# Optimization experiments

Hardware: AMD Instinct MI355X
Metric: run time of the kernel (lower is better)

The kernel has to match this reference:

```python
import jax, jax.numpy as jnp
import numpy as np

COMMITMENT_COST = 0.25


def setup_inputs() -> dict:
    key = jax.random.key(0)
    k1, k2 = jax.random.split(key)
    x = jax.random.normal(k1, (4, 64, 32, 32, 32), dtype=jnp.float32)
    weight = jax.random.normal(k2, (512, 64), dtype=jnp.float32)
    return {"x": x, "weight": weight}


def reference(x, weight):
    b, c, h, w, d = x.shape  # c == embed_dim
    # [b, h, w, d, c] -> [N, c]
    flat = jnp.transpose(x, (0, 2, 3, 4, 1)).reshape(-1, c)
    # squared L2 distances to each codebook vector: [N, n_embed]
    distances = (
        jnp.sum(flat * flat, axis=1, keepdims=True)
        - 2.0 * (flat @ weight.T)
        + jnp.sum(weight * weight, axis=1)
    )
    embed_idx_flat = jnp.argmin(distances, axis=1)  # == argmax(-distances)
    embed_idx = embed_idx_flat.reshape(b, h, w, d)
    # gather codebook rows and move embed dim back to channel position
    quantized = jnp.transpose(weight[embed_idx], (0, 4, 1, 2, 3))  # [b, c, h, w, d]
    latent_loss = COMMITMENT_COST * jnp.mean(
        (jax.lax.stop_gradient(quantized) - x) ** 2
    )
    quantized_st = jax.lax.stop_gradient(quantized - x) + x
    return quantized_st, embed_idx, latent_loss
```

## Files before the change

### kernel.cpp

```cpp
#include <hip/hip_runtime.h>
#include <hip/hip_bf16.h>

#define HWD      32768
#define NC       64
#define NE       512
#define OUT_IDX  8388608
#define OUT_LOSS 8519680

#define WS_WSQ_F   16
#define WS_WP_B    4096
#define WS_NEEDED  200704

typedef __attribute__((ext_vector_type(8))) short bf16x8;
typedef __attribute__((ext_vector_type(4))) float f32x4;

__device__ inline unsigned short bf16_rne(float v) {
    unsigned u = __builtin_bit_cast(unsigned, v);
    return (unsigned short)((u + 0x7FFFu + ((u >> 16) & 1u)) >> 16);
}
__device__ inline float bf16_f(unsigned short s) {
    return __builtin_bit_cast(float, (unsigned)s << 16);
}
__device__ inline void split3(float v, unsigned short& h, unsigned short& m,
                              unsigned short& l) {
    h = bf16_rne(v);
    float r1 = v - bf16_f(h);
    m = bf16_rne(r1);
    float r2 = r1 - bf16_f(m);
    l = bf16_rne(r2);
}

__global__ __launch_bounds__(256) void vq_prep(
    const float* __restrict__ w, float* __restrict__ ws)
{
    const int gtid = blockIdx.x * 256 + threadIdx.x;
    if (gtid == 0) { ws[0] = 0.f; ((unsigned*)ws)[1] = 0u; }
    if (gtid < NE) {
        const float4* row = (const float4*)(w + (size_t)gtid * NC);
        float s0 = 0.f, s1 = 0.f, s2 = 0.f, s3 = 0.f;
#pragma unroll
        for (int k = 0; k < 16; ++k) {
            float4 v = row[k];
            s0 = fmaf(v.x, v.x, s0); s1 = fmaf(v.y, v.y, s1);
            s2 = fmaf(v.z, v.z, s2); s3 = fmaf(v.w, v.w, s3);
        }
        ws[WS_WSQ_F + gtid] = (s0 + s1) + (s2 + s3);
    }
    const int lane_s = gtid & 63;
    int t = gtid >> 6;
    const int plane = t % 3; t /= 3;
    const int kc = t & 1;
    const int ct = t >> 1;
    const int code = ct * 16 + (lane_s & 15);
    const int kb   = kc * 32 + (lane_s >> 4) * 8;
    const float* src = w + (size_t)code * NC + kb;
    unsigned short o[8];
#pragma unroll
    for (int j = 0; j < 8; ++j) {
        unsigned short h, m, l;
        split3(src[j], h, m, l);
        o[j] = (plane == 0) ? h : (plane == 1) ? m : l;
    }
    unsigned short* dst = (unsigned short*)((char*)ws + WS_WP_B) + (size_t)gtid * 8;
#pragma unroll
    for (int j = 0; j < 8; ++j) dst[j] = o[j];
}

__global__ __launch_bounds__(256, 4) void vq_fused2(
    const float* __restrict__ x, const float* __restrict__ w,
    float* __restrict__ ws, float* __restrict__ out)
{
    __shared__ float q_sh[64 * 65];
    __shared__ int   idx_sh[128];
    __shared__ float wred[4];

    const int tid    = threadIdx.x;
    const int wv     = tid >> 6;
    const int lane   = tid & 63;
    const int lanelo = lane & 15;
    const int quad   = lane >> 4;
    const int posB   = blockIdx.x * 128;
    const int b      = posB >> 15;
    const int hwdB   = posB & (HWD - 1);
    const size_t xoff = (size_t)b * NC * HWD + hwdB;
    const int wpos   = wv * 32;

    bf16x8 A[2][2][3];
    float  xsqp[2];
#pragma unroll
    for (int pt = 0; pt < 2; ++pt) {
        float xs = 0.f;
#pragma unroll
        for (int kc = 0; kc < 2; ++kc) {
            bf16x8 fh, fm, fl;
#pragma unroll
            for (int j = 0; j < 8; ++j) {
                const int k = kc * 32 + quad * 8 + j;
                const float v = x[xoff + (size_t)k * HWD + wpos + pt * 16 + lanelo];
                unsigned short h, m, l;
                split3(v, h, m, l);
                fh[j] = (short)h; fm[j] = (short)m; fl[j] = (short)l;
                xs = fmaf(v, v, xs);
            }
            A[pt][kc][0] = fh; A[pt][kc][1] = fm; A[pt][kc][2] = fl;
        }
        xs += __shfl_xor(xs, 16);
        xs += __shfl_xor(xs, 32);
        xsqp[pt] = xs;
    }
    float xsq_r[2][4];
#pragma unroll
    for (int pt = 0; pt < 2; ++pt)
#pragma unroll
        for (int r = 0; r < 4; ++r)
            xsq_r[pt][r] = __shfl(xsqp[pt], quad * 4 + r);

    const bf16x8* wp   = (const bf16x8*)((const char*)ws + WS_WP_B);
    const float*  wsqp = ws + WS_WSQ_F;

    float best[2][4];
    int   bidx[2][4];
#pragma unroll
    for (int pt = 0; pt < 2; ++pt)
#pragma unroll
        for (int r = 0; r < 4; ++r) { best[pt][r] = 3.402823466e38f; bidx[pt][r] = 0; }

    for (int ct = 0; ct < 32; ++ct) {
        bf16x8 B[2][3];
#pragma unroll
        for (int kc = 0; kc < 2; ++kc)
#pragma unroll
            for (int p = 0; p < 3; ++p)
                B[kc][p] = wp[(size_t)((ct * 2 + kc) * 3 + p) * 64 + lane];
        const float wsq_c = wsqp[ct * 16 + lanelo];

#pragma unroll
        for (int pt = 0; pt < 2; ++pt) {
            f32x4 acc = {0.f, 0.f, 0.f, 0.f};
            acc = __builtin_amdgcn_mfma_f32_16x16x32_bf16(A[pt][0][2], B[0][0], acc, 0, 0, 0);
            acc = __builtin_amdgcn_mfma_f32_16x16x32_bf16(A[pt][1][2], B[1][0], acc, 0, 0, 0);
            acc = __builtin_amdgcn_mfma_f32_16x16x32_bf16(A[pt][0][1], B[0][1], acc, 0, 0, 0);
            acc = __builtin_amdgcn_mfma_f32_16x16x32_bf16(A[pt][1][1], B[1][1], acc, 0, 0, 0);
            acc = __builtin_amdgcn_mfma_f32_16x16x32_bf16(A[pt][0][0], B[0][2], acc, 0, 0, 0);
            acc = __builtin_amdgcn_mfma_f32_16x16x32_bf16(A[pt][1][0], B[1][2], acc, 0, 0, 0);
            acc = __builtin_amdgcn_mfma_f32_16x16x32_bf16(A[pt][0][1], B[0][0], acc, 0, 0, 0);
            acc = __builtin_amdgcn_mfma_f32_16x16x32_bf16(A[pt][1][1], B[1][0], acc, 0, 0, 0);
            acc = __builtin_amdgcn_mfma_f32_16x16x32_bf16(A[pt][0][0], B[0][1], acc, 0, 0, 0);
            acc = __builtin_amdgcn_mfma_f32_16x16x32_bf16(A[pt][1][0], B[1][1], acc, 0, 0, 0);
            acc = __builtin_amdgcn_mfma_f32_16x16x32_bf16(A[pt][0][0], B[0][0], acc, 0, 0, 0);
            acc = __builtin_amdgcn_mfma_f32_16x16x32_bf16(A[pt][1][0], B[1][0], acc, 0, 0, 0);
#pragma unroll
            for (int r = 0; r < 4; ++r) {
                const float d = fmaf(-2.f, acc[r], xsq_r[pt][r]) + wsq_c;
                const int ge = ct * 16 + lanelo;
                if (d < best[pt][r]) { best[pt][r] = d; bidx[pt][r] = ge; }
            }
        }
    }

#pragma unroll
    for (int pt = 0; pt < 2; ++pt)
#pragma unroll
        for (int r = 0; r < 4; ++r) {
            float d = best[pt][r]; int i = bidx[pt][r];
#pragma unroll
            for (int mlane = 1; mlane <= 8; mlane <<= 1) {
                const float d2 = __shfl_xor(d, mlane);
                const int   i2 = __shfl_xor(i, mlane);
                if (d2 < d || (d2 == d && i2 < i)) { d = d2; i = i2; }
            }
            if (lanelo == 0)
                idx_sh[wpos + pt * 16 + quad * 4 + r] = i;
        }
    __syncthreads();

    if (tid < 128) out[OUT_IDX + posB + tid] = (float)idx_sh[tid];

    float lsum = 0.f;
#pragma unroll 1
    for (int rnd = 0; rnd < 2; ++rnd) {
        if (rnd) __syncthreads();
#pragma unroll
        for (int it = 0; it < 16; ++it) {
            const int e = it * 256 + tid;
            const int r = e >> 6, c = e & 63;
            q_sh[r * 65 + c] = w[(size_t)idx_sh[rnd * 64 + r] * NC + c];
        }
        __syncthreads();
#pragma unroll
        for (int it = 0; it < 16; ++it) {
            const int e = it * 256 + tid;
            const int c = e >> 6;
            const int p = e & 63;
            const size_t off = xoff + (size_t)c * HWD + rnd * 64 + p;
            const float xv = x[off];
            const float q  = q_sh[p * 65 + c];
            const float dq = q - xv;
            lsum = fmaf(dq, dq, lsum);
            out[off] = dq + xv;
        }
    }

#pragma unroll
    for (int off = 32; off >= 1; off >>= 1) lsum += __shfl_down(lsum, off);
    if (lane == 0) wred[wv] = lsum;
    __syncthreads();
    if (tid == 0) {
        atomicAdd((float*)ws, (wred[0] + wred[1]) + (wred[2] + wred[3]));
        __threadfence();
        const unsigned done = atomicAdd((unsigned*)ws + 1, 1u);
        if (done == 1023u) {
            const float L = atomicAdd((float*)ws, 0.f);
            out[OUT_LOSS] = 0.25f * L / 8388608.0f;
        }
    }
}

__global__ __launch_bounds__(256, 2) void vq_fused_fb(
    const float* __restrict__ x, const float* __restrict__ w,
    float* __restrict__ out, float* __restrict__ loss_acc)
{
    __shared__ float lw[256 * NC];
    __shared__ float wsq[256];
    __shared__ float wred[4];
    const int tid = threadIdx.x;
    const int n0  = blockIdx.x * 512;
    const int b   = n0 >> 15;
    const int hwd = (n0 & (HWD - 1)) + tid;
    const float* xp = x + (size_t)b * NC * HWD + hwd;
    float xr0[NC], xr1[NC];
#pragma unroll
    for (int c = 0; c < NC; ++c) { xr0[c] = xp[(size_t)c * HWD]; xr1[c] = xp[(size_t)c * HWD + 256]; }
    float xsq0 = 0.f, xsq1 = 0.f;
#pragma unroll
    for (int c = 0; c < NC; ++c) { xsq0 = fmaf(xr0[c], xr0[c], xsq0); xsq1 = fmaf(xr1[c], xr1[c], xsq1); }
    float best0 = 3.402823466e38f, best1 = 3.402823466e38f;
    int bi0 = 0, bi1 = 0;
    for (int pass = 0; pass < 2; ++pass) {
        if (pass) __syncthreads();
        const float4* wt = (const float4*)(w + pass * 256 * NC);
        float4* l4 = (float4*)lw;
#pragma unroll
        for (int k = 0; k < 16; ++k) l4[tid + k * 256] = wt[tid + k * 256];
        {
            const float4* row = wt + tid * 16;
            float s0 = 0.f, s1 = 0.f, s2 = 0.f, s3 = 0.f;
#pragma unroll
            for (int k = 0; k < 16; ++k) {
                float4 v = row[k];
                s0 = fmaf(v.x, v.x, s0); s1 = fmaf(v.y, v.y, s1);
                s2 = fmaf(v.z, v.z, s2); s3 = fmaf(v.w, v.w, s3);
            }
            wsq[tid] = (s0 + s1) + (s2 + s3);
        }
        __syncthreads();
#pragma unroll 2
        for (int e = 0; e < 256; ++e) {
            const float4* row = (const float4*)(lw + e * NC);
            float a0 = 0.f, a1 = 0.f, c0 = 0.f, c1 = 0.f;
#pragma unroll
            for (int k = 0; k < 16; ++k) {
                float4 v = row[k];
                a0 = fmaf(xr0[4 * k + 0], v.x, a0); a1 = fmaf(xr0[4 * k + 1], v.y, a1);
                a0 = fmaf(xr0[4 * k + 2], v.z, a0); a1 = fmaf(xr0[4 * k + 3], v.w, a1);
                c0 = fmaf(xr1[4 * k + 0], v.x, c0); c1 = fmaf(xr1[4 * k + 1], v.y, c1);
                c0 = fmaf(xr1[4 * k + 2], v.z, c0); c1 = fmaf(xr1[4 * k + 3], v.w, c1);
            }
            const float d0 = (xsq0 - 2.f * (a0 + a1)) + wsq[e];
            const float d1 = (xsq1 - 2.f * (c0 + c1)) + wsq[e];
            const int ge = pass * 256 + e;
            if (d0 < best0) { best0 = d0; bi0 = ge; }
            if (d1 < best1) { best1 = d1; bi1 = ge; }
        }
    }
    float* o0 = out + (size_t)b * NC * HWD + hwd;
    float lsum = 0.f;
    const float4* r0 = (const float4*)(w + bi0 * NC);
    const float4* r1 = (const float4*)(w + bi1 * NC);
#pragma unroll
    for (int k = 0; k < 16; ++k) {
        float4 q0 = r0[k], q1 = r1[k];
        float qv0[4] = { q0.x, q0.y, q0.z, q0.w };
        float qv1[4] = { q1.x, q1.y, q1.z, q1.w };
#pragma unroll
        for (int j = 0; j < 4; ++j) {
            const int c = 4 * k + j;
            const float dv0 = qv0[j] - xr0[c];
            const float dv1 = qv1[j] - xr1[c];
            lsum = fmaf(dv0, dv0, lsum); lsum = fmaf(dv1, dv1, lsum);
            o0[(size_t)c * HWD] = dv0 + xr0[c];
            o0[(size_t)c * HWD + 256] = dv1 + xr1[c];
        }
    }
    const int n = b * HWD + hwd;
    out[OUT_IDX + n] = (float)bi0;
    out[OUT_IDX + n + 256] = (float)bi1;
#pragma unroll
    for (int off = 32; off >= 1; off >>= 1) lsum += __shfl_down(lsum, off);
    if ((tid & 63) == 0) wred[tid >> 6] = lsum;
    __syncthreads();
    if (tid == 0) atomicAdd(loss_acc, (wred[0] + wred[1]) + (wred[2] + wred[3]));
}

__global__ void vq_loss_fin_fb(const float* __restrict__ acc, float* __restrict__ out)
{
    out[OUT_LOSS] = 0.25f * acc[0] / 8388608.0f;
}

extern "C" void kernel_launch(void* const* d_in, const int* in_sizes, int n_in,
                              void* d_out, int out_size, void* d_ws, size_t ws_size,
                              hipStream_t stream)
{
    const float* x = (const float*)d_in[0];
    const float* w = (const float*)d_in[1];
    float* out = (float*)d_out;
    float* ws  = (float*)d_ws;

    if (ws_size >= WS_NEEDED) {
        vq_prep<<<48, 256, 0, stream>>>(w, ws);
        vq_fused2<<<1024, 256, 0, stream>>>(x, w, ws, out);
    } else {
        hipMemsetAsync(d_ws, 0, sizeof(float), stream);
        vq_fused_fb<<<256, 256, 0, stream>>>(x, w, out, ws);
        vq_loss_fin_fb<<<1, 1, 0, stream>>>(ws, out);
    }
}
```

Measured before the change: 162.0 us.

## Double-buffer codebook tile loads and drop per-row x-norm from argmin

The codebook-tile loop now uses two register buffers, loading the next tile's B fragments and weight norms while the MFMA chain on the current tile runs, so global-load latency overlaps with compute. It also drops the ||x||^2 term from the distance, since it is constant per row and cannot change the argmin, which removes the squared-sum, shuffles and per-element adds. The recorded best distance no longer includes ||x||^2, so any later code that reads best values would see different numbers. Extra B registers could raise register pressure under the 4-wave launch bound.

```diff
diff --git a/kernel.cpp b/kernel.cpp
--- a/kernel.cpp
+++ b/kernel.cpp
@@ -64,6 +64,48 @@
     unsigned short* dst = (unsigned short*)((char*)ws + WS_WP_B) + (size_t)gtid * 8;
 #pragma unroll
     for (int j = 0; j < 8; ++j) dst[j] = o[j];
+}
+
+__device__ __forceinline__ void loadB(const bf16x8* __restrict__ wp,
+                                      const float* __restrict__ wsqp,
+                                      const int ct, const int lane,
+                                      const int lanelo,
+                                      bf16x8 B[2][3], float& wsq)
+{
+#pragma unroll
+    for (int kc = 0; kc < 2; ++kc)
+#pragma unroll
+        for (int p = 0; p < 3; ++p)
+            B[kc][p] = wp[(size_t)((ct * 2 + kc) * 3 + p) * 64 + lane];
+    wsq = wsqp[ct * 16 + lanelo];
+}
+
+__device__ __forceinline__ void tileUpd(const bf16x8 A[2][2][3],
+                                        const bf16x8 B[2][3], const float wsq,
+                                        const int ct, const int lanelo,
+                                        float best[2][4], int bidx[2][4])
+{
+#pragma unroll
+    for (int pt = 0; pt < 2; ++pt) {
+        f32x4 acc = {0.f, 0.f, 0.f, 0.f};
+        acc = __builtin_amdgcn_mfma_f32_16x16x32_bf16(A[pt][0][2], B[0][0], acc, 0, 0, 0);
+        acc = __builtin_amdgcn_mfma_f32_16x16x32_bf16(A[pt][1][2], B[1][0], acc, 0, 0, 0);
+        acc = __builtin_amdgcn_mfma_f32_16x16x32_bf16(A[pt][0][1], B[0][1], acc, 0, 0, 0);
+        acc = __builtin_amdgcn_mfma_f32_16x16x32_bf16(A[pt][1][1], B[1][1], acc, 0, 0, 0);
+        acc = __builtin_amdgcn_mfma_f32_16x16x32_bf16(A[pt][0][0], B[0][2], acc, 0, 0, 0);
+        acc = __builtin_amdgcn_mfma_f32_16x16x32_bf16(A[pt][1][0], B[1][2], acc, 0, 0, 0);
+        acc = __builtin_amdgcn_mfma_f32_16x16x32_bf16(A[pt][0][1], B[0][0], acc, 0, 0, 0);
+        acc = __builtin_amdgcn_mfma_f32_16x16x32_bf16(A[pt][1][1], B[1][0], acc, 0, 0, 0);
+        acc = __builtin_amdgcn_mfma_f32_16x16x32_bf16(A[pt][0][0], B[0][1], acc, 0, 0, 0);
+        acc = __builtin_amdgcn_mfma_f32_16x16x32_bf16(A[pt][1][0], B[1][1], acc, 0, 0, 0);
+        acc = __builtin_amdgcn_mfma_f32_16x16x32_bf16(A[pt][0][0], B[0][0], acc, 0, 0, 0);
+        acc = __builtin_amdgcn_mfma_f32_16x16x32_bf16(A[pt][1][0], B[1][0], acc, 0, 0, 0);
+#pragma unroll
+        for (int r = 0; r < 4; ++r) {
+            const float d = fmaf(-2.f, acc[r], wsq);
+            if (d < best[pt][r]) { best[pt][r] = d; bidx[pt][r] = ct * 16 + lanelo; }
+        }
+    }
 }
 
 __global__ __launch_bounds__(256, 4) void vq_fused2(
@@ -85,11 +127,16 @@
     const size_t xoff = (size_t)b * NC * HWD + hwdB;
     const int wpos   = wv * 32;
 
+    const bf16x8* wp   = (const bf16x8*)((const char*)ws + WS_WP_B);
+    const float*  wsqp = ws + WS_WSQ_F;
+
+    bf16x8 B0[2][3], B1[2][3];
+    float  w0, w1;
+    loadB(wp, wsqp, 0, lane, lanelo, B0, w0);
+
     bf16x8 A[2][2][3];
-    float  xsqp[2];
 #pragma unroll
     for (int pt = 0; pt < 2; ++pt) {
-        float xs = 0.f;
 #pragma unroll
         for (int kc = 0; kc < 2; ++kc) {
             bf16x8 fh, fm, fl;
@@ -100,23 +147,10 @@
                 unsigned short h, m, l;
                 split3(v, h, m, l);
                 fh[j] = (short)h; fm[j] = (short)m; fl[j] = (short)l;
-                xs = fmaf(v, v, xs);
             }
             A[pt][kc][0] = fh; A[pt][kc][1] = fm; A[pt][kc][2] = fl;
         }
-        xs += __shfl_xor(xs, 16);
-        xs += __shfl_xor(xs, 32);
-        xsqp[pt] = xs;
-    }
-    float xsq_r[2][4];
-#pragma unroll
-    for (int pt = 0; pt < 2; ++pt)
-#pragma unroll
-        for (int r = 0; r < 4; ++r)
-            xsq_r[pt][r] = __shfl(xsqp[pt], quad * 4 + r);
-
-    const bf16x8* wp   = (const bf16x8*)((const char*)ws + WS_WP_B);
-    const float*  wsqp = ws + WS_WSQ_F;
+    }
 
     float best[2][4];
     int   bidx[2][4];
@@ -125,37 +159,13 @@
 #pragma unroll
         for (int r = 0; r < 4; ++r) { best[pt][r] = 3.402823466e38f; bidx[pt][r] = 0; }
 
-    for (int ct = 0; ct < 32; ++ct) {
-        bf16x8 B[2][3];
-#pragma unroll
-        for (int kc = 0; kc < 2; ++kc)
-#pragma unroll
-            for (int p = 0; p < 3; ++p)
-                B[kc][p] = wp[(size_t)((ct * 2 + kc) * 3 + p) * 64 + lane];
-        const float wsq_c = wsqp[ct * 16 + lanelo];
-
-#pragma unroll
-        for (int pt = 0; pt < 2; ++pt) {
-            f32x4 acc = {0.f, 0.f, 0.f, 0.f};
-            acc = __builtin_amdgcn_mfma_f32_16x16x32_bf16(A[pt][0][2], B[0][0], acc, 0, 0, 0);
-            acc = __builtin_amdgcn_mfma_f32_16x16x32_bf16(A[pt][1][2], B[1][0], acc, 0, 0, 0);
-            acc = __builtin_amdgcn_mfma_f32_16x16x32_bf16(A[pt][0][1], B[0][1], acc, 0, 0, 0);
-            acc = __builtin_amdgcn_mfma_f32_16x16x32_bf16(A[pt][1][1], B[1][1], acc, 0, 0, 0);
-            acc = __builtin_amdgcn_mfma_f32_16x16x32_bf16(A[pt][0][0], B[0][2], acc, 0, 0, 0);
-            acc = __builtin_amdgcn_mfma_f32_16x16x32_bf16(A[pt][1][0], B[1][2], acc, 0, 0, 0);
-            acc = __builtin_amdgcn_mfma_f32_16x16x32_bf16(A[pt][0][1], B[0][0], acc, 0, 0, 0);
-            acc = __builtin_amdgcn_mfma_f32_16x16x32_bf16(A[pt][1][1], B[1][0], acc, 0, 0, 0);
-            acc = __builtin_amdgcn_mfma_f32_16x16x32_bf16(A[pt][0][0], B[0][1], acc, 0, 0, 0);
-            acc = __builtin_amdgcn_mfma_f32_16x16x32_bf16(A[pt][1][0], B[1][1], acc, 0, 0, 0);
-            acc = __builtin_amdgcn_mfma_f32_16x16x32_bf16(A[pt][0][0], B[0][0], acc, 0, 0, 0);
-            acc = __builtin_amdgcn_mfma_f32_16x16x32_bf16(A[pt][1][0], B[1][0], acc, 0, 0, 0);
-#pragma unroll
-            for (int r = 0; r < 4; ++r) {
-                const float d = fmaf(-2.f, acc[r], xsq_r[pt][r]) + wsq_c;
-                const int ge = ct * 16 + lanelo;
-                if (d < best[pt][r]) { best[pt][r] = d; bidx[pt][r] = ge; }
-            }
-        }
+#pragma unroll 1
+    for (int ct2 = 0; ct2 < 16; ++ct2) {
+        const int ce = ct2 * 2;
+        loadB(wp, wsqp, ce + 1, lane, lanelo, B1, w1);
+        tileUpd(A, B0, w0, ce, lanelo, best, bidx);
+        loadB(wp, wsqp, (ce + 2) & 31, lane, lanelo, B0, w0);
+        tileUpd(A, B1, w1, ce + 1, lanelo, best, bidx);
     }
 
 #pragma unroll
```

Result: slower. 173.7 us (+7.2%).
